# Performance work log

Measured on AMD Instinct MI355X. Metric: run time of the kernel, lower is better.

Reference implementation:

```python
import jax, jax.numpy as jnp
import numpy as np

N_HEADS = 16
HEAD_DIM = 64
HIDDEN = N_HEADS * HEAD_DIM


def setup_inputs() -> dict:
    key = jax.random.key(0)
    ks = jax.random.split(key, 10)
    B, F, T = 2, 2048, 2048
    std = 0.02
    inp = {
        "from_tensor": jax.random.normal(ks[0], (B, F, HIDDEN), dtype=jnp.float32),
        "to_tensor": jax.random.normal(ks[1], (B, T, HIDDEN), dtype=jnp.float32),
        "attention_mask": jax.random.randint(ks[2], (B, F, T), 0, 2, dtype=jnp.int32),
        "Wq": jax.random.normal(ks[3], (HIDDEN, HIDDEN), dtype=jnp.float32) * std,
        "bq": jnp.zeros((HIDDEN,), dtype=jnp.float32),
        "Wk": jax.random.normal(ks[4], (HIDDEN, HIDDEN), dtype=jnp.float32) * std,
        "bk": jnp.zeros((HIDDEN,), dtype=jnp.float32),
        "Wv": jax.random.normal(ks[5], (HIDDEN, HIDDEN), dtype=jnp.float32) * std,
        "bv": jnp.zeros((HIDDEN,), dtype=jnp.float32),
    }
    return inp


def reference(from_tensor, to_tensor, attention_mask, Wq, bq, Wk, bk, Wv, bv):
    B, F, _ = from_tensor.shape
    T = to_tensor.shape[1]
    N, H = N_HEADS, HEAD_DIM

    # QKV projections (no activations: query/key/value act fns are None)
    q = (from_tensor @ Wq + bq).reshape(B, F, N, H)
    k = (to_tensor @ Wk + bk).reshape(B, T, N, H)
    v = (to_tensor @ Wv + bv).reshape(B, T, N, H)

    scores = jnp.einsum('BFNH,BTNH->BNFT', q, k) * (1.0 / np.sqrt(float(H)))
    # additive mask: mask [B,F,T] -> [B,1,F,T]; 0 entries get -10000
    adder = (1.0 - attention_mask.astype(jnp.float32))[:, None, :, :] * -10000.0
    scores = scores + adder
    probs = jax.nn.softmax(scores, axis=-1)  # dropout skipped (inference)

    context = jnp.einsum('BNFT,BTNH->BFNH', probs, v)
    return context.reshape(B, F, N * H)
```

## Files before the change

### kernel.cpp

```cpp
#include <hip/hip_runtime.h>


typedef short v8s __attribute__((ext_vector_type(8)));
typedef float v4f __attribute__((ext_vector_type(4)));
typedef unsigned short u16;
typedef unsigned int   u32;
typedef unsigned long long u64;

constexpr float QSCALE = 0.18033688011112042f;

__device__ __forceinline__ u16 f2bf(float f) {
    u32 u = __builtin_bit_cast(u32, f);
    u += 0x7fffu + ((u >> 16) & 1u);
    return (u16)(u >> 16);
}

__device__ __forceinline__ u32 pack_trunc(float a, float b) {
    return __builtin_amdgcn_perm(__builtin_bit_cast(u32, b),
                                 __builtin_bit_cast(u32, a), 0x07060302u);
}

__device__ __forceinline__ v8s ld8(const u16* p) {
    return *reinterpret_cast<const v8s*>(p);
}

__global__ __launch_bounds__(256) void prep(
    const float* __restrict__ from, const float* __restrict__ to,
    u16* __restrict__ Xf, u16* __restrict__ Xt,
    const float* __restrict__ Wq, const float* __restrict__ Wk, const float* __restrict__ Wv,
    u16* __restrict__ Wqt, u16* __restrict__ Wkt, u16* __restrict__ Wvt,
    const int* __restrict__ mask, u64* __restrict__ words) {
    __shared__ float tile[32][33];
    const int bid = blockIdx.x, tid = threadIdx.x;
    if (bid < 8192) {
        int i = bid * 256 + tid;
        const float4* s;
        ushort4* d;
        int j;
        if (i < 1048576) { s = (const float4*)from; d = (ushort4*)Xf; j = i; }
        else             { s = (const float4*)to;   d = (ushort4*)Xt; j = i - 1048576; }
        float4 v = s[j];
        ushort4 o;
        o.x = f2bf(v.x); o.y = f2bf(v.y); o.z = f2bf(v.z); o.w = f2bf(v.w);
        d[j] = o;
    } else if (bid < 11264) {
        const int r = bid - 8192;
        const int zz = r >> 10, rem = r & 1023;
        const float* W = zz == 0 ? Wq : (zz == 1 ? Wk : Wv);
        u16* Wt = zz == 0 ? Wqt : (zz == 1 ? Wkt : Wvt);
        const int tx = tid & 31, ty = tid >> 5;
        const int n0 = (rem & 31) * 32, k0 = (rem >> 5) * 32;
        for (int i = 0; i < 4; i++)
            tile[ty + i * 8][tx] = W[(size_t)(k0 + ty + i * 8) * 1024 + n0 + tx];
        __syncthreads();
        for (int i = 0; i < 4; i++)
            Wt[(size_t)(n0 + ty + i * 8) * 1024 + k0 + tx] = f2bf(tile[tx][ty + i * 8]);
    } else {
        int g = (bid - 11264) * 256 + tid;
        int w = g >> 6, lane = g & 63;
        int v = mask[(size_t)w * 64 + lane];
        u64 bits = __ballot(v != 0);
        if (lane == 0) words[w] = bits;
    }
}

__global__ __launch_bounds__(256) void gemm_qkv(
    const u16* __restrict__ Xf, const u16* __restrict__ Xt,
    const u16* __restrict__ Wqt, const u16* __restrict__ Wkt, const u16* __restrict__ Wvt,
    const float* __restrict__ bq, const float* __restrict__ bk, const float* __restrict__ bv,
    u16* __restrict__ Qb, u16* __restrict__ Kb, u16* __restrict__ Vtb) {
    const int z = blockIdx.z;
    const u16* A      = z == 0 ? Xf : Xt;
    const u16* Bt     = z == 0 ? Wqt : (z == 1 ? Wkt : Wvt);
    const float* bias = z == 0 ? bq : (z == 1 ? bk : bv);
    u16* C            = z == 0 ? Qb : (z == 1 ? Kb : Vtb);
    const int mode    = (z == 2);
    const float sc    = (z == 0) ? QSCALE : 1.0f;

    __shared__ u16 As[2][128][32];
    __shared__ u16 Bs[2][128][32];
    const uint4* Ag = reinterpret_cast<const uint4*>(A);
    const uint4* Bg = reinterpret_cast<const uint4*>(Bt);

    const int tid = threadIdx.x;
    const int lane = tid & 63, wave = tid >> 6;
    const int quad = lane >> 4, l16 = lane & 15;
    const int wm = wave >> 1, wn = wave & 1;
    const int m0 = blockIdx.x * 128, n0 = blockIdx.y * 128;

    const int cg  = (lane & 3) ^ ((lane >> 3) & 3);
    const int sw8 = (quad ^ ((l16 >> 1) & 3)) * 8;

    const int gi0 = wave * 4;
    const uint4 *ap0, *ap1, *ap2, *ap3, *bp0, *bp1, *bp2, *bp3;
    {
        const int rl = lane >> 2;
        const int rb0 = ((gi0 + 0) & 7) * 16 + rl, kh0 = (gi0 + 0) >> 3;
        const int rb1 = ((gi0 + 1) & 7) * 16 + rl, kh1 = (gi0 + 1) >> 3;
        const int rb2 = ((gi0 + 2) & 7) * 16 + rl, kh2 = (gi0 + 2) >> 3;
        const int rb3 = ((gi0 + 3) & 7) * 16 + rl, kh3 = (gi0 + 3) >> 3;
        ap0 = Ag + (size_t)(m0 + rb0) * 128 + kh0 * 4 + cg;
        ap1 = Ag + (size_t)(m0 + rb1) * 128 + kh1 * 4 + cg;
        ap2 = Ag + (size_t)(m0 + rb2) * 128 + kh2 * 4 + cg;
        ap3 = Ag + (size_t)(m0 + rb3) * 128 + kh3 * 4 + cg;
        bp0 = Bg + (size_t)(n0 + rb0) * 128 + kh0 * 4 + cg;
        bp1 = Bg + (size_t)(n0 + rb1) * 128 + kh1 * 4 + cg;
        bp2 = Bg + (size_t)(n0 + rb2) * 128 + kh2 * 4 + cg;
        bp3 = Bg + (size_t)(n0 + rb3) * 128 + kh3 * 4 + cg;
    }
    uint4* da = reinterpret_cast<uint4*>((u16*)As + gi0 * 512) + lane;
    uint4* db = reinterpret_cast<uint4*>((u16*)Bs + gi0 * 512) + lane;

    v4f acc[4][4];
    for (int i = 0; i < 4; i++)
        for (int j = 0; j < 4; j++) acc[i][j] = (v4f)0.0f;

    uint4 sa0 = *ap0; ap0 += 8;
    uint4 sa1 = *ap1; ap1 += 8;
    uint4 sa2 = *ap2; ap2 += 8;
    uint4 sa3 = *ap3; ap3 += 8;
    uint4 sb0 = *bp0; bp0 += 8;
    uint4 sb1 = *bp1; bp1 += 8;
    uint4 sb2 = *bp2; bp2 += 8;
    uint4 sb3 = *bp3; bp3 += 8;

    for (int k0 = 0; k0 < 16; k0++) {
        __syncthreads();
        da[0]   = sa0;  da[64]  = sa1;  da[128] = sa2;  da[192] = sa3;
        db[0]   = sb0;  db[64]  = sb1;  db[128] = sb2;  db[192] = sb3;
        __syncthreads();

        if (k0 < 15) {
            sa0 = *ap0; ap0 += 8;
            sa1 = *ap1; ap1 += 8;
            sa2 = *ap2; ap2 += 8;
            sa3 = *ap3; ap3 += 8;
            sb0 = *bp0; bp0 += 8;
            sb1 = *bp1; bp1 += 8;
            sb2 = *bp2; bp2 += 8;
            sb3 = *bp3; bp3 += 8;
        }

        #pragma unroll
        for (int kk = 0; kk < 2; kk++) {
            v8s af[4], bf[4];
            #pragma unroll
            for (int mt = 0; mt < 4; mt++) af[mt] = ld8(&As[kk][wm * 64 + mt * 16 + l16][sw8]);
            #pragma unroll
            for (int nt = 0; nt < 4; nt++) bf[nt] = ld8(&Bs[kk][wn * 64 + nt * 16 + l16][sw8]);
            #pragma unroll
            for (int mt = 0; mt < 4; mt++)
                #pragma unroll
                for (int nt = 0; nt < 4; nt++)
                    acc[mt][nt] = __builtin_amdgcn_mfma_f32_16x16x32_bf16(af[mt], bf[nt], acc[mt][nt], 0, 0, 0);
        }
    }

    #pragma unroll
    for (int nt = 0; nt < 4; nt++) {
        const int col = n0 + wn * 64 + nt * 16 + l16;
        const float bvv = bias[col];
        #pragma unroll
        for (int mt = 0; mt < 4; mt++) {
            const int mbase = m0 + wm * 64 + mt * 16 + quad * 4;
            if (mode == 0) {
                for (int r = 0; r < 4; r++)
                    C[(size_t)(mbase + r) * 1024 + col] = f2bf((acc[mt][nt][r] + bvv) * sc);
            } else {
                const int b = mbase >> 11, t = mbase & 2047;
                const int head = col >> 6, h = col & 63;
                ushort4 pk;
                pk.x = f2bf(acc[mt][nt][0] + bvv);
                pk.y = f2bf(acc[mt][nt][1] + bvv);
                pk.z = f2bf(acc[mt][nt][2] + bvv);
                pk.w = f2bf(acc[mt][nt][3] + bvv);
                *reinterpret_cast<ushort4*>(&C[(size_t)((b * 16 + head) * 64 + h) * 2048 + t]) = pk;
            }
        }
    }
}

__global__ __launch_bounds__(512, 4) void attn_fused(
    const u16* __restrict__ Qb, const u16* __restrict__ Kb,
    const u16* __restrict__ Vtb, const u64* __restrict__ mw,
    float* __restrict__ out) {
    __shared__ u16 Ks[2][2][64][32];
    __shared__ u16 Vs[2][2][64][32];
    __shared__ u32 Ps[8 * 1152];

    const int tid = threadIdx.x;
    const int lane = tid & 63, wave = tid >> 6;
    const int quad = lane >> 4, l16 = lane & 15;
    const int fwave = wave & 3, tw = wave >> 2;
    const int b = blockIdx.x >> 4, head = blockIdx.x & 15;
    const int f0 = blockIdx.y * 128;

    const uint4* Kg = reinterpret_cast<const uint4*>(Kb);
    const uint4* Vg = reinterpret_cast<const uint4*>(Vtb);
    const size_t vbase4 = (size_t)(b * 16 + head) * 64 * 256;

    const int cg  = (lane & 3) ^ ((lane >> 3) & 3);
    const int sw8 = (quad ^ ((l16 >> 1) & 3)) * 8;

    v8s qf[2][2];
    #pragma unroll
    for (int kk = 0; kk < 2; kk++)
        #pragma unroll
        for (int qh = 0; qh < 2; qh++)
            qf[kk][qh] = ld8(Qb + ((size_t)(b * 2048 + f0 + fwave * 32 + qh * 16 + l16) * 16 + head) * 64
                                + kk * 32 + quad * 8);

    v8s ones;
    #pragma unroll
    for (int i = 0; i < 8; i++) ones[i] = (short)0x3F80;

    const uint4 *sp0, *sp1, *sp2, *sp3;
    u16 *sd;
    size_t sinc;
    {
        const int rl = lane >> 2;
        if (wave < 4) {
            const int g0 = wave * 4;
            sd = (u16*)Ks + g0 * 512;
            sinc = 8192;
            #define KPTR(g) (Kg + ((size_t)(b * 2048 + ((g) >> 3) * 1024 + ((g) & 3) * 16 + rl) * 16 + head) * 8 \
                                + (((g) >> 2) & 1) * 4 + cg)
            sp0 = KPTR(g0); sp1 = KPTR(g0 + 1); sp2 = KPTR(g0 + 2); sp3 = KPTR(g0 + 3);
            #undef KPTR
        } else {
            const int g0 = (wave - 4) * 4;
            sd = (u16*)Vs + g0 * 512;
            sinc = 8;
            #define VPTR(g) (Vg + vbase4 + (size_t)(((g) & 3) * 16 + rl) * 256 + ((g) >> 3) * 128 \
                                + (((g) >> 2) & 1) * 4 + cg)
            sp0 = VPTR(g0); sp1 = VPTR(g0 + 1); sp2 = VPTR(g0 + 2); sp3 = VPTR(g0 + 3);
            #undef VPTR
        }
    }
    uint4* sd4 = reinterpret_cast<uint4*>(sd) + lane;

    v4f accO[2][4], accL[2];
    #pragma unroll
    for (int qh = 0; qh < 2; qh++) {
        accL[qh] = (v4f)0.0f;
        for (int ht = 0; ht < 4; ht++) accO[qh][ht] = (v4f)0.0f;
    }

    u32* myPs = Ps + wave * 1152;
    const u64* mrow = mw + (size_t)(b * 2048 + f0 + fwave * 32 + l16) * 32 + tw * 16;

    uint4 st0 = *sp0; sp0 += sinc;
    uint4 st1 = *sp1; sp1 += sinc;
    uint4 st2 = *sp2; sp2 += sinc;
    uint4 st3 = *sp3; sp3 += sinc;

    for (int it = 0; it < 16; it++) {
        __syncthreads();
        sd4[0]   = st0;
        sd4[64]  = st1;
        sd4[128] = st2;
        sd4[192] = st3;
        __syncthreads();

        if (it < 15) {
            st0 = *sp0; sp0 += sinc;
            st1 = *sp1; sp1 += sinc;
            st2 = *sp2; sp2 += sinc;
            st3 = *sp3; sp3 += sinc;
        }

        v4f s[2][4];
        #pragma unroll
        for (int qh = 0; qh < 2; qh++)
            for (int mt = 0; mt < 4; mt++) s[qh][mt] = (v4f)0.0f;
        #pragma unroll
        for (int kk = 0; kk < 2; kk++) {
            v8s kf[4];
            #pragma unroll
            for (int mt = 0; mt < 4; mt++) kf[mt] = ld8(&Ks[tw][kk][mt * 16 + l16][sw8]);
            #pragma unroll
            for (int qh = 0; qh < 2; qh++)
                #pragma unroll
                for (int mt = 0; mt < 4; mt++)
                    s[qh][mt] = __builtin_amdgcn_mfma_f32_16x16x32_bf16(kf[mt], qf[kk][qh], s[qh][mt], 0, 0, 0);
        }

        u32 pk[2][8];
        #pragma unroll
        for (int qh = 0; qh < 2; qh++) {
            const u64 w = mrow[qh * 512 + it];
            const u32 lo = (u32)(w >> (quad * 4));
            const u32 hi = (u32)(w >> (quad * 4 + 32));
            #pragma unroll
            for (int mt = 0; mt < 4; mt++) {
                const u32 bits = ((mt & 2) ? hi : lo) >> ((mt & 1) * 16);
                float p[4];
                #pragma unroll
                for (int r = 0; r < 4; r++) {
                    const float e = __builtin_amdgcn_exp2f(s[qh][mt][r]);
                    p[r] = ((bits >> r) & 1u) ? e : 0.0f;
                }
                pk[qh][mt * 2]     = pack_trunc(p[0], p[1]);
                pk[qh][mt * 2 + 1] = pack_trunc(p[2], p[3]);
            }
        }

        #pragma unroll
        for (int qh = 0; qh < 2; qh++) {
            const int row = qh * 16 + l16;
            #pragma unroll
            for (int mt = 0; mt < 4; mt++)
                *reinterpret_cast<uint2*>(&myPs[row * 36 + mt * 8 + quad * 2]) =
                    make_uint2(pk[qh][mt * 2], pk[qh][mt * 2 + 1]);
        }

        #pragma unroll
        for (int kk = 0; kk < 2; kk++) {
            v8s vf[4];
            #pragma unroll
            for (int ht = 0; ht < 4; ht++) vf[ht] = ld8(&Vs[tw][kk][ht * 16 + l16][sw8]);
            #pragma unroll
            for (int qh = 0; qh < 2; qh++) {
                const v8s pf = *reinterpret_cast<const v8s*>(
                    &myPs[(qh * 16 + l16) * 36 + kk * 16 + quad * 4]);
                #pragma unroll
                for (int ht = 0; ht < 4; ht++)
                    accO[qh][ht] = __builtin_amdgcn_mfma_f32_16x16x32_bf16(vf[ht], pf, accO[qh][ht], 0, 0, 0);
                accL[qh] = __builtin_amdgcn_mfma_f32_16x16x32_bf16(ones, pf, accL[qh], 0, 0, 0);
            }
        }
    }

    __syncthreads();
    float* fb = (float*)Ps;
    if (tw == 1) {
        float* wdst = fb + fwave * 2304 + lane * 36;
        #pragma unroll
        for (int qh = 0; qh < 2; qh++)
            #pragma unroll
            for (int ht = 0; ht < 4; ht++)
                *reinterpret_cast<v4f*>(wdst + (qh * 4 + ht) * 4) = accO[qh][ht];
        wdst[32] = accL[0][0];
        wdst[33] = accL[1][0];
    }
    __syncthreads();
    if (tw == 0) {
        const float* rsrc = fb + fwave * 2304 + lane * 36;
        float inv[2];
        #pragma unroll
        for (int qh = 0; qh < 2; qh++)
            inv[qh] = 1.0f / (accL[qh][0] + rsrc[32 + qh]);
        #pragma unroll
        for (int qh = 0; qh < 2; qh++) {
            const size_t ro = (size_t)(b * 2048 + f0 + fwave * 32 + qh * 16 + l16) * 1024 + head * 64;
            #pragma unroll
            for (int ht = 0; ht < 4; ht++) {
                const v4f p = *reinterpret_cast<const v4f*>(rsrc + (qh * 4 + ht) * 4);
                float4 o;
                o.x = (accO[qh][ht][0] + p[0]) * inv[qh];
                o.y = (accO[qh][ht][1] + p[1]) * inv[qh];
                o.z = (accO[qh][ht][2] + p[2]) * inv[qh];
                o.w = (accO[qh][ht][3] + p[3]) * inv[qh];
                *reinterpret_cast<float4*>(&out[ro + ht * 16 + quad * 4]) = o;
            }
        }
    }
}

extern "C" void kernel_launch(void* const* d_in, const int* in_sizes, int n_in,
                              void* d_out, int out_size, void* d_ws, size_t ws_size,
                              hipStream_t stream) {
    const float* from = (const float*)d_in[0];
    const float* to   = (const float*)d_in[1];
    const int*   mask = (const int*)d_in[2];
    const float* Wq = (const float*)d_in[3];
    const float* bq = (const float*)d_in[4];
    const float* Wk = (const float*)d_in[5];
    const float* bk = (const float*)d_in[6];
    const float* Wv = (const float*)d_in[7];
    const float* bv = (const float*)d_in[8];
    float* out = (float*)d_out;

    u16* Xf  = (u16*)d_ws;
    u16* Xt  = Xf  + 4194304;
    u16* Wqt = Xt  + 4194304;
    u16* Wkt = Wqt + 1048576;
    u16* Wvt = Wkt + 1048576;
    u16* Qb  = Wvt + 1048576;
    u16* Kb  = Qb  + 4194304;
    u16* Vtb = Kb  + 4194304;
    u64* mwords = (u64*)(Vtb + 4194304);

    prep<<<44032, 256, 0, stream>>>(from, to, Xf, Xt, Wq, Wk, Wv, Wqt, Wkt, Wvt, mask, mwords);

    gemm_qkv<<<dim3(32, 8, 3), 256, 0, stream>>>(Xf, Xt, Wqt, Wkt, Wvt, bq, bk, bv, Qb, Kb, Vtb);

    attn_fused<<<dim3(32, 16), 512, 0, stream>>>(Qb, Kb, Vtb, mwords, out);
}
```

Baseline: 213.5 us.

## Fuse fp32-to-bf16 activation conversion into QKV GEMM loads and batch mask packing

Removes the separate pass that converted from/to activations to bf16 in the prep kernel. The GEMM now loads fp32 activations directly, rounds them to bf16 in registers, and writes them to shared memory, which avoids a full write and re-read of the bf16 copies. The mask-packing blocks now each process 8 words per wave, which shrinks the prep grid. GEMM launch bounds now request 3 blocks per CU. The cost is that the GEMM's A-operand global traffic doubles, and the extra conversion ALU work plus held registers may add pressure.

```diff
diff --git a/kernel.cpp b/kernel.cpp
--- a/kernel.cpp
+++ b/kernel.cpp
@@ -20,32 +20,33 @@
                                  __builtin_bit_cast(u32, a), 0x07060302u);
 }
 
+__device__ __forceinline__ u32 pack_rnd(u32 ua, u32 ub) {
+    ua += 0x7fffu + ((ua >> 16) & 1u);
+    ub += 0x7fffu + ((ub >> 16) & 1u);
+    return __builtin_amdgcn_perm(ub, ua, 0x07060302u);
+}
+
+__device__ __forceinline__ uint4 cvt8(uint4 lo, uint4 hi) {
+    uint4 r;
+    r.x = pack_rnd(lo.x, lo.y);
+    r.y = pack_rnd(lo.z, lo.w);
+    r.z = pack_rnd(hi.x, hi.y);
+    r.w = pack_rnd(hi.z, hi.w);
+    return r;
+}
+
 __device__ __forceinline__ v8s ld8(const u16* p) {
     return *reinterpret_cast<const v8s*>(p);
 }
 
 __global__ __launch_bounds__(256) void prep(
-    const float* __restrict__ from, const float* __restrict__ to,
-    u16* __restrict__ Xf, u16* __restrict__ Xt,
     const float* __restrict__ Wq, const float* __restrict__ Wk, const float* __restrict__ Wv,
     u16* __restrict__ Wqt, u16* __restrict__ Wkt, u16* __restrict__ Wvt,
     const int* __restrict__ mask, u64* __restrict__ words) {
     __shared__ float tile[32][33];
     const int bid = blockIdx.x, tid = threadIdx.x;
-    if (bid < 8192) {
-        int i = bid * 256 + tid;
-        const float4* s;
-        ushort4* d;
-        int j;
-        if (i < 1048576) { s = (const float4*)from; d = (ushort4*)Xf; j = i; }
-        else             { s = (const float4*)to;   d = (ushort4*)Xt; j = i - 1048576; }
-        float4 v = s[j];
-        ushort4 o;
-        o.x = f2bf(v.x); o.y = f2bf(v.y); o.z = f2bf(v.z); o.w = f2bf(v.w);
-        d[j] = o;
-    } else if (bid < 11264) {
-        const int r = bid - 8192;
-        const int zz = r >> 10, rem = r & 1023;
+    if (bid < 3072) {
+        const int zz = bid >> 10, rem = bid & 1023;
         const float* W = zz == 0 ? Wq : (zz == 1 ? Wk : Wv);
         u16* Wt = zz == 0 ? Wqt : (zz == 1 ? Wkt : Wvt);
         const int tx = tid & 31, ty = tid >> 5;
@@ -56,21 +57,25 @@
         for (int i = 0; i < 4; i++)
             Wt[(size_t)(n0 + ty + i * 8) * 1024 + k0 + tx] = f2bf(tile[tx][ty + i * 8]);
     } else {
-        int g = (bid - 11264) * 256 + tid;
-        int w = g >> 6, lane = g & 63;
-        int v = mask[(size_t)w * 64 + lane];
-        u64 bits = __ballot(v != 0);
-        if (lane == 0) words[w] = bits;
-    }
-}
-
-__global__ __launch_bounds__(256) void gemm_qkv(
-    const u16* __restrict__ Xf, const u16* __restrict__ Xt,
+        const int lane = tid & 63;
+        const int g0 = (bid - 3072) * 32 + (tid >> 6) * 8;
+        const int* mp = mask + (size_t)g0 * 64 + lane;
+        u64* wp = words + g0;
+        #pragma unroll
+        for (int i = 0; i < 8; i++) {
+            const u64 bits = __ballot(mp[(size_t)i * 64] != 0);
+            if (lane == 0) wp[i] = bits;
+        }
+    }
+}
+
+__global__ __launch_bounds__(256, 3) void gemm_qkv(
+    const float* __restrict__ Xf32, const float* __restrict__ Xt32,
     const u16* __restrict__ Wqt, const u16* __restrict__ Wkt, const u16* __restrict__ Wvt,
     const float* __restrict__ bq, const float* __restrict__ bk, const float* __restrict__ bv,
     u16* __restrict__ Qb, u16* __restrict__ Kb, u16* __restrict__ Vtb) {
     const int z = blockIdx.z;
-    const u16* A      = z == 0 ? Xf : Xt;
+    const float* A    = z == 0 ? Xf32 : Xt32;
     const u16* Bt     = z == 0 ? Wqt : (z == 1 ? Wkt : Wvt);
     const float* bias = z == 0 ? bq : (z == 1 ? bk : bv);
     u16* C            = z == 0 ? Qb : (z == 1 ? Kb : Vtb);
@@ -99,10 +104,10 @@
         const int rb1 = ((gi0 + 1) & 7) * 16 + rl, kh1 = (gi0 + 1) >> 3;
         const int rb2 = ((gi0 + 2) & 7) * 16 + rl, kh2 = (gi0 + 2) >> 3;
         const int rb3 = ((gi0 + 3) & 7) * 16 + rl, kh3 = (gi0 + 3) >> 3;
-        ap0 = Ag + (size_t)(m0 + rb0) * 128 + kh0 * 4 + cg;
-        ap1 = Ag + (size_t)(m0 + rb1) * 128 + kh1 * 4 + cg;
-        ap2 = Ag + (size_t)(m0 + rb2) * 128 + kh2 * 4 + cg;
-        ap3 = Ag + (size_t)(m0 + rb3) * 128 + kh3 * 4 + cg;
+        ap0 = Ag + (size_t)(m0 + rb0) * 256 + (kh0 * 4 + cg) * 2;
+        ap1 = Ag + (size_t)(m0 + rb1) * 256 + (kh1 * 4 + cg) * 2;
+        ap2 = Ag + (size_t)(m0 + rb2) * 256 + (kh2 * 4 + cg) * 2;
+        ap3 = Ag + (size_t)(m0 + rb3) * 256 + (kh3 * 4 + cg) * 2;
         bp0 = Bg + (size_t)(n0 + rb0) * 128 + kh0 * 4 + cg;
         bp1 = Bg + (size_t)(n0 + rb1) * 128 + kh1 * 4 + cg;
         bp2 = Bg + (size_t)(n0 + rb2) * 128 + kh2 * 4 + cg;
@@ -115,26 +120,30 @@
     for (int i = 0; i < 4; i++)
         for (int j = 0; j < 4; j++) acc[i][j] = (v4f)0.0f;
 
-    uint4 sa0 = *ap0; ap0 += 8;
-    uint4 sa1 = *ap1; ap1 += 8;
-    uint4 sa2 = *ap2; ap2 += 8;
-    uint4 sa3 = *ap3; ap3 += 8;
+    uint4 a0l = ap0[0], a0h = ap0[1]; ap0 += 16;
+    uint4 a1l = ap1[0], a1h = ap1[1]; ap1 += 16;
+    uint4 a2l = ap2[0], a2h = ap2[1]; ap2 += 16;
+    uint4 a3l = ap3[0], a3h = ap3[1]; ap3 += 16;
     uint4 sb0 = *bp0; bp0 += 8;
     uint4 sb1 = *bp1; bp1 += 8;
     uint4 sb2 = *bp2; bp2 += 8;
     uint4 sb3 = *bp3; bp3 += 8;
+    uint4 ca0 = cvt8(a0l, a0h);
+    uint4 ca1 = cvt8(a1l, a1h);
+    uint4 ca2 = cvt8(a2l, a2h);
+    uint4 ca3 = cvt8(a3l, a3h);
 
     for (int k0 = 0; k0 < 16; k0++) {
         __syncthreads();
-        da[0]   = sa0;  da[64]  = sa1;  da[128] = sa2;  da[192] = sa3;
+        da[0]   = ca0;  da[64]  = ca1;  da[128] = ca2;  da[192] = ca3;
         db[0]   = sb0;  db[64]  = sb1;  db[128] = sb2;  db[192] = sb3;
         __syncthreads();
 
         if (k0 < 15) {
-            sa0 = *ap0; ap0 += 8;
-            sa1 = *ap1; ap1 += 8;
-            sa2 = *ap2; ap2 += 8;
-            sa3 = *ap3; ap3 += 8;
+            a0l = ap0[0]; a0h = ap0[1]; ap0 += 16;
+            a1l = ap1[0]; a1h = ap1[1]; ap1 += 16;
+            a2l = ap2[0]; a2h = ap2[1]; ap2 += 16;
+            a3l = ap3[0]; a3h = ap3[1]; ap3 += 16;
             sb0 = *bp0; bp0 += 8;
             sb1 = *bp1; bp1 += 8;
             sb2 = *bp2; bp2 += 8;
@@ -153,6 +162,13 @@
                 #pragma unroll
                 for (int nt = 0; nt < 4; nt++)
                     acc[mt][nt] = __builtin_amdgcn_mfma_f32_16x16x32_bf16(af[mt], bf[nt], acc[mt][nt], 0, 0, 0);
+        }
+
+        if (k0 < 15) {
+            ca0 = cvt8(a0l, a0h);
+            ca1 = cvt8(a1l, a1h);
+            ca2 = cvt8(a2l, a2h);
+            ca3 = cvt8(a3l, a3h);
         }
     }
 
@@ -381,9 +397,7 @@
     const float* bv = (const float*)d_in[8];
     float* out = (float*)d_out;
 
-    u16* Xf  = (u16*)d_ws;
-    u16* Xt  = Xf  + 4194304;
-    u16* Wqt = Xt  + 4194304;
+    u16* Wqt = (u16*)d_ws;
     u16* Wkt = Wqt + 1048576;
     u16* Wvt = Wkt + 1048576;
     u16* Qb  = Wvt + 1048576;
@@ -391,9 +405,10 @@
     u16* Vtb = Kb  + 4194304;
     u64* mwords = (u64*)(Vtb + 4194304);
 
-    prep<<<44032, 256, 0, stream>>>(from, to, Xf, Xt, Wq, Wk, Wv, Wqt, Wkt, Wvt, mask, mwords);
-
-    gemm_qkv<<<dim3(32, 8, 3), 256, 0, stream>>>(Xf, Xt, Wqt, Wkt, Wvt, bq, bk, bv, Qb, Kb, Vtb);
+    prep<<<7168, 256, 0, stream>>>(Wq, Wk, Wv, Wqt, Wkt, Wvt, mask, mwords);
+
+    gemm_qkv<<<dim3(32, 8, 3), 256, 0, stream>>>(from, to, Wqt, Wkt, Wvt, bq, bk, bv,
+                                                 Qb, Kb, Vtb);
 
     attn_fused<<<dim3(32, 16), 512, 0, stream>>>(Qb, Kb, Vtb, mwords, out);
 }
```

Result: no change. 212.6 us, median of 2 (-0.4%).
